# Kernel tuning notes

Measured on AMD Instinct MI355X. Metric: run time of the kernel, lower is better.

Reference implementation:

```python
import jax, jax.numpy as jnp
import numpy as np

N = 50000   # nodes
E = 800000  # edges
D = 128     # input feature dim
HID = 64    # hidden dim
NEG_SLOPE = 0.2


def setup_inputs() -> dict:
    key = jax.random.key(0)
    ks = jax.random.split(key, 12)
    s = 0.1
    x = jax.random.normal(ks[0], (N, D), jnp.float32)
    edge_index = jax.random.randint(ks[1], (2, E), 0, N, dtype=jnp.int64)
    # layer 1: GATConv(128 -> 64, heads=2, concat=False)
    W1 = jax.random.normal(ks[2], (D, 2 * HID), jnp.float32) * s
    a_src1 = jax.random.normal(ks[3], (2, HID), jnp.float32) * s
    a_dst1 = jax.random.normal(ks[4], (2, HID), jnp.float32) * s
    b1 = jnp.zeros((HID,), jnp.float32)
    # layer 2: GATConv(64 -> 64, heads=1, concat=False)
    W2 = jax.random.normal(ks[5], (HID, HID), jnp.float32) * s
    a_src2 = jax.random.normal(ks[6], (1, HID), jnp.float32) * s
    a_dst2 = jax.random.normal(ks[7], (1, HID), jnp.float32) * s
    b2 = jnp.zeros((HID,), jnp.float32)
    # classifier Linear(64 -> 2)
    Wc = jax.random.normal(ks[8], (HID, 2), jnp.float32) * s
    bc = jnp.zeros((2,), jnp.float32)
    return {"x": x, "edge_index": edge_index, "W1": W1, "a_src1": a_src1,
            "a_dst1": a_dst1, "b1": b1, "W2": W2, "a_src2": a_src2,
            "a_dst2": a_dst2, "b2": b2, "Wc": Wc, "bc": bc}


def _gat_layer(x, src, dst, W, a_s, a_d, b, n):
    """PyG GATConv (concat=False -> mean over heads), eval mode."""
    H, C = a_s.shape
    h = (x @ W).reshape(n, H, C)                      # [N,H,C]
    alpha_s = jnp.sum(h * a_s, axis=-1)               # [N,H]
    alpha_d = jnp.sum(h * a_d, axis=-1)               # [N,H]
    e = jax.nn.leaky_relu(alpha_s[src] + alpha_d[dst], NEG_SLOPE)  # [E,H]
    # segment softmax over incoming edges of each target node
    m = jax.ops.segment_max(e, dst, num_segments=n)   # [N,H]
    e = jnp.exp(e - m[dst])
    denom = jax.ops.segment_sum(e, dst, num_segments=n)
    alpha = e / (denom[dst] + 1e-16)                  # [E,H]
    msg = h[src] * alpha[:, :, None]                  # [E,H,C]
    out = jax.ops.segment_sum(msg, dst, num_segments=n)  # [N,H,C]
    return out.mean(axis=1) + b                       # [N,C]


def reference(x, edge_index, W1, a_src1, a_dst1, b1, W2, a_src2, a_dst2, b2, Wc, bc):
    n = x.shape[0]
    loops = jnp.arange(n, dtype=edge_index.dtype)     # PyG add_self_loops=True
    src = jnp.concatenate([edge_index[0], loops])
    dst = jnp.concatenate([edge_index[1], loops])
    h = jax.nn.elu(_gat_layer(x, src, dst, W1, a_src1, a_dst1, b1, n))
    h = jax.nn.elu(_gat_layer(h, src, dst, W2, a_src2, a_dst2, b2, n))
    logits = h @ Wc + bc
    return jax.nn.log_softmax(logits, axis=1)
```

## Files before the change

kernel.cpp:

```cpp
#include <hip/hip_runtime.h>
#include <math.h>

#define NN 50000
#define NE 800000
#define NT (NE + NN)
#define NBUCK 196
#define BE 4096
#define NBLK_B ((NT + BE - 1) / BE)
#define CAP 6144
#define NBLK_G ((NN + 63) / 64)

typedef short bf16x8 __attribute__((ext_vector_type(8)));
typedef float f32x4 __attribute__((ext_vector_type(4)));
union U16x8 { uint4 u; bf16x8 s; };

__device__ __forceinline__ unsigned pk_bf16x2(float x, float y) {
  unsigned ux = __float_as_uint(x); ux = ux + 0x7FFFu + ((ux >> 16) & 1u);
  unsigned uy = __float_as_uint(y); uy = uy + 0x7FFFu + ((uy >> 16) & 1u);
  return (ux >> 16) | (uy & 0xFFFF0000u);
}
__device__ __forceinline__ unsigned short bf16_1(float x) {
  unsigned u = __float_as_uint(x); u = u + 0x7FFFu + ((u >> 16) & 1u);
  return (unsigned short)(u >> 16);
}
__device__ __forceinline__ float blo(unsigned v) { return __uint_as_float(v << 16); }
__device__ __forceinline__ float bhi(unsigned v) { return __uint_as_float(v & 0xFFFF0000u); }

__global__ __launch_bounds__(256) void k_prep(const float* __restrict__ W1, const float* __restrict__ W2,
                                              unsigned short* __restrict__ w1f,
                                              unsigned short* __restrict__ w2f,
                                              int* __restrict__ bcur) {
  int i = blockIdx.x * 256 + threadIdx.x;
  if (i < NBUCK) bcur[i] = i * CAP;
  if (i < 128 * 128) {
    int k = i >> 7, col = i & 127;
    int ct = col >> 4, kt = k >> 5, lane = (((k >> 3) & 3) << 4) | (col & 15), j = k & 7;
    w1f[(((ct << 2) | kt) * 64 + lane) * 8 + j] = bf16_1(W1[i]);
  } else if (i < 128 * 128 + 64 * 64) {
    int e = i - 128 * 128;
    int k = e >> 6, col = e & 63;
    int ct = col >> 4, kt = k >> 5, lane = (((k >> 3) & 3) << 4) | (col & 15), j = k & 7;
    w2f[(((ct << 1) | kt) * 64 + lane) * 8 + j] = bf16_1(W2[e]);
  }
}

__global__ __launch_bounds__(256) void k_gb(
    const int* __restrict__ src, const int* __restrict__ dst,
    int* __restrict__ bcur, unsigned* __restrict__ staging,
    const float* __restrict__ x, const unsigned short* __restrict__ w1f,
    const float* __restrict__ asw_g, const float* __restrict__ adw_g,
    unsigned short* __restrict__ h1b, float* __restrict__ as1, float* __restrict__ ad1) {
  __shared__ int hist[NBUCK];
  __shared__ int base[NBUCK];
  if (blockIdx.x < NBLK_B) {
    const int t = threadIdx.x;
    const int e0 = blockIdx.x * BE;
    if (t < NBUCK) hist[t] = 0;
    __syncthreads();
    for (int j = t; j < BE; j += 256) {
      int i = e0 + j;
      if (i >= NT) break;
      int d = (i < NE) ? dst[i] : (i - NE);
      atomicAdd(&hist[d >> 8], 1);
    }
    __syncthreads();
    if (t < NBUCK) {
      int c = hist[t];
      base[t] = c ? atomicAdd(&bcur[t], c) : 0;
      hist[t] = 0;
    }
    __syncthreads();
    for (int j = t; j < BE; j += 256) {
      int i = e0 + j;
      if (i >= NT) break;
      int s, d;
      if (i < NE) { s = src[i]; d = dst[i]; } else { s = d = i - NE; }
      int b = d >> 8;
      int off = atomicAdd(&hist[b], 1);
      staging[base[b] + off] = ((unsigned)d << 16) | (unsigned)s;
    }
    return;
  }
  const int bid = blockIdx.x - NBLK_B;
  const int t = threadIdx.x;
  const int wid = t >> 6, l = t & 63;
  const int lr = l & 15, lg = l >> 4;
  const int arow = bid * 64 + wid * 16 + lr;
  const bool aok = arow < NN;

  float asw_t[8], adw_t[8];
#pragma unroll
  for (int ct = 0; ct < 8; ++ct) {
    asw_t[ct] = asw_g[ct * 16 + lr];
    adw_t[ct] = adw_g[ct * 16 + lr];
  }

  f32x4 acc[8];
#pragma unroll
  for (int ct = 0; ct < 8; ++ct) acc[ct] = (f32x4){0.f, 0.f, 0.f, 0.f};

#pragma unroll
  for (int kt = 0; kt < 4; ++kt) {
    U16x8 a;
    if (aok) {
      const float* xp = &x[(long long)arow * 128 + kt * 32 + lg * 8];
      float4 f0 = *(const float4*)xp;
      float4 f1 = *(const float4*)(xp + 4);
      a.u.x = pk_bf16x2(f0.x, f0.y); a.u.y = pk_bf16x2(f0.z, f0.w);
      a.u.z = pk_bf16x2(f1.x, f1.y); a.u.w = pk_bf16x2(f1.z, f1.w);
    } else {
      a.u = make_uint4(0, 0, 0, 0);
    }
#pragma unroll
    for (int ct = 0; ct < 8; ++ct) {
      U16x8 b;
      b.u = *(const uint4*)&w1f[(((ct << 2) | kt) * 64 + l) * 8];
      acc[ct] = __builtin_amdgcn_mfma_f32_16x16x32_bf16(a.s, b.s, acc[ct], 0, 0, 0);
    }
  }

  const int gr0 = bid * 64 + wid * 16 + lg * 4;
#pragma unroll
  for (int reg = 0; reg < 4; ++reg) {
    int grow = gr0 + reg;
    bool ok = grow < NN;
    float s0 = 0.f, s1 = 0.f, d0 = 0.f, d1 = 0.f;
#pragma unroll
    for (int ct = 0; ct < 8; ++ct) {
      float v = acc[ct][reg];
      if (ok) h1b[(long long)grow * 128 + ct * 16 + lr] = bf16_1(v);
      if (ct < 4) { s0 += v * asw_t[ct]; d0 += v * adw_t[ct]; }
      else        { s1 += v * asw_t[ct]; d1 += v * adw_t[ct]; }
    }
#pragma unroll
    for (int off = 1; off < 16; off <<= 1) {
      s0 += __shfl_xor(s0, off); d0 += __shfl_xor(d0, off);
      s1 += __shfl_xor(s1, off); d1 += __shfl_xor(d1, off);
    }
    if (ok && lr == 0) {
      as1[grow * 2] = s0; as1[grow * 2 + 1] = s1;
      ad1[grow * 2] = d0; ad1[grow * 2 + 1] = d1;
    }
  }
}

__global__ __launch_bounds__(256) void k_scatter2(const unsigned* __restrict__ staging,
                                                  const int* __restrict__ bcur,
                                                  int* __restrict__ rowptr,
                                                  unsigned short* __restrict__ csr16) {
  __shared__ int lcnt[256];
  __shared__ int wsum[4];
  __shared__ int sOff, sTot;
  const int b = blockIdx.x;
  const int t = threadIdx.x;
  const int nlo = b << 8;
  const int l = t & 63, w = t >> 6;

  int bc = (t < NBUCK) ? bcur[t] - t * CAP : 0;
  int sc = bc;
#pragma unroll
  for (int off = 1; off < 64; off <<= 1) {
    int u = __shfl_up(sc, off);
    if (l >= off) sc += u;
  }
  if (l == 63) wsum[w] = sc;
  __syncthreads();
  {
    int wo = 0;
    for (int i = 0; i < w; ++i) wo += wsum[i];
    int incl = sc + wo;
    if (t == b) sOff = incl - bc;
    if (t == 255) sTot = incl;
  }
  lcnt[t] = 0;
  __syncthreads();

  const int s0 = b * CAP;
  const int cnt = bcur[b] - s0;
  for (int k = t; k < cnt; k += 256)
    atomicAdd(&lcnt[(int)(staging[s0 + k] >> 16) - nlo], 1);
  __syncthreads();
  int v = lcnt[t];
  int sc2 = v;
#pragma unroll
  for (int off = 1; off < 64; off <<= 1) {
    int u = __shfl_up(sc2, off);
    if (l >= off) sc2 += u;
  }
  __syncthreads();
  if (l == 63) wsum[w] = sc2;
  __syncthreads();
  int wo = 0;
  for (int i = 0; i < w; ++i) wo += wsum[i];
  const int base = sOff + sc2 + wo - v;
  if (nlo + t < NN) rowptr[nlo + t] = base;
  if (b == NBUCK - 1 && t == 0) rowptr[NN] = sTot;
  __syncthreads();
  lcnt[t] = base;
  __syncthreads();
  for (int k = t; k < cnt; k += 256) {
    unsigned e = staging[s0 + k];
    int d = (int)(e >> 16) - nlo;
    int pos = atomicAdd(&lcnt[d], 1);
    csr16[pos] = (unsigned short)(e & 0xFFFFu);
  }
}

__global__ __launch_bounds__(256) void k_gat1(
    const int* __restrict__ rowptr, const unsigned short* __restrict__ csr16,
    const uint2* __restrict__ h1x2, const float2* __restrict__ as1,
    const float2* __restrict__ ad1, const float* __restrict__ b1,
    uint2* __restrict__ out1x2) {
  __shared__ float4 sw[4][2][64];
  const int t = threadIdx.x;
  const int wv = t >> 6;
  const int p = t & 63;
  const int hw = p >> 5;
  const int l = p & 31;
  const int n = blockIdx.x * 8 + wv * 2 + hw;
  if (n >= NN) return;
  const int beg = rowptr[n], end = rowptr[n + 1];
  const int deg = end - beg;
  const float2 adn = ad1[n];
  const int hd = l >> 4;

  float a0 = 0.f, a1 = 0.f, a2 = 0.f, a3 = 0.f;
  float inv;

  if (deg <= 64) {
    int sA = 0, sB = 0;
    float e0A = -1e30f, e1A = -1e30f, e0B = -1e30f, e1B = -1e30f;
    if (l < deg) {
      sA = csr16[beg + l];
      float2 a = as1[sA];
      e0A = a.x + adn.x; e0A = fmaxf(e0A, 0.2f * e0A);
      e1A = a.y + adn.y; e1A = fmaxf(e1A, 0.2f * e1A);
    }
    if (l + 32 < deg) {
      sB = csr16[beg + l + 32];
      float2 a = as1[sB];
      e0B = a.x + adn.x; e0B = fmaxf(e0B, 0.2f * e0B);
      e1B = a.y + adn.y; e1B = fmaxf(e1B, 0.2f * e1B);
    }
    float m0 = fmaxf(e0A, e0B), m1 = fmaxf(e1A, e1B);
#pragma unroll
    for (int off = 1; off < 32; off <<= 1) {
      m0 = fmaxf(m0, __shfl_xor(m0, off));
      m1 = fmaxf(m1, __shfl_xor(m1, off));
    }
    float w0A = (l < deg) ? __expf(e0A - m0) : 0.f;
    float w1A = (l < deg) ? __expf(e1A - m1) : 0.f;
    float w0B = (l + 32 < deg) ? __expf(e0B - m0) : 0.f;
    float w1B = (l + 32 < deg) ? __expf(e1B - m1) : 0.f;
    float d0 = w0A + w0B, d1 = w1A + w1B;
#pragma unroll
    for (int off = 1; off < 32; off <<= 1) {
      d0 += __shfl_xor(d0, off);
      d1 += __shfl_xor(d1, off);
    }
    sw[wv][hw][l]      = make_float4(__int_as_float(sA), w0A, w1A, 0.f);
    sw[wv][hw][l + 32] = make_float4(__int_as_float(sB), w0B, w1B, 0.f);
    __builtin_amdgcn_wave_barrier();
    inv = 1.f / ((hd ? d1 : d0) + 1e-16f);

    int j = 0;
    for (; j + 8 <= deg; j += 8) {
      float4 a[8]; uint2 v[8];
#pragma unroll
      for (int u = 0; u < 8; ++u) a[u] = sw[wv][hw][j + u];
#pragma unroll
      for (int u = 0; u < 8; ++u) v[u] = h1x2[(__float_as_int(a[u].x) << 5) + l];
#pragma unroll
      for (int u = 0; u < 8; ++u) {
        float wgt = hd ? a[u].z : a[u].y;
        a0 += wgt * blo(v[u].x); a1 += wgt * bhi(v[u].x);
        a2 += wgt * blo(v[u].y); a3 += wgt * bhi(v[u].y);
      }
    }
    if (j + 4 <= deg) {
      float4 a[4]; uint2 v[4];
#pragma unroll
      for (int u = 0; u < 4; ++u) a[u] = sw[wv][hw][j + u];
#pragma unroll
      for (int u = 0; u < 4; ++u) v[u] = h1x2[(__float_as_int(a[u].x) << 5) + l];
#pragma unroll
      for (int u = 0; u < 4; ++u) {
        float wgt = hd ? a[u].z : a[u].y;
        a0 += wgt * blo(v[u].x); a1 += wgt * bhi(v[u].x);
        a2 += wgt * blo(v[u].y); a3 += wgt * bhi(v[u].y);
      }
      j += 4;
    }
    for (; j < deg; ++j) {
      float4 a = sw[wv][hw][j];
      uint2 v = h1x2[(__float_as_int(a.x) << 5) + l];
      float wgt = hd ? a.z : a.y;
      a0 += wgt * blo(v.x); a1 += wgt * bhi(v.x);
      a2 += wgt * blo(v.y); a3 += wgt * bhi(v.y);
    }
  } else {
    float m0 = -1e30f, d0 = 0.f, m1 = -1e30f, d1 = 0.f;
    for (int k = beg + l; k < end; k += 32) {
      float2 a = as1[csr16[k]];
      float e0 = a.x + adn.x; e0 = fmaxf(e0, 0.2f * e0);
      float e1 = a.y + adn.y; e1 = fmaxf(e1, 0.2f * e1);
      if (e0 > m0) { d0 *= __expf(m0 - e0); m0 = e0; }
      d0 += __expf(e0 - m0);
      if (e1 > m1) { d1 *= __expf(m1 - e1); m1 = e1; }
      d1 += __expf(e1 - m1);
    }
#pragma unroll
    for (int off = 1; off < 32; off <<= 1) {
      float mo = __shfl_xor(m0, off), dd = __shfl_xor(d0, off);
      float mn = fmaxf(m0, mo);
      d0 = d0 * __expf(m0 - mn) + dd * __expf(mo - mn);
      m0 = mn;
      mo = __shfl_xor(m1, off); dd = __shfl_xor(d1, off);
      mn = fmaxf(m1, mo);
      d1 = d1 * __expf(m1 - mn) + dd * __expf(mo - mn);
      m1 = mn;
    }
    inv = 1.f / ((hd ? d1 : d0) + 1e-16f);
    for (int c0 = beg; c0 < end; c0 += 64) {
      int nc = end - c0; if (nc > 64) nc = 64;
      int sA = 0, sB = 0; float w0A = 0.f, w1A = 0.f, w0B = 0.f, w1B = 0.f;
      if (l < nc) {
        sA = csr16[c0 + l];
        float2 a = as1[sA];
        float e0 = a.x + adn.x; e0 = fmaxf(e0, 0.2f * e0);
        float e1 = a.y + adn.y; e1 = fmaxf(e1, 0.2f * e1);
        w0A = __expf(e0 - m0); w1A = __expf(e1 - m1);
      }
      if (l + 32 < nc) {
        sB = csr16[c0 + l + 32];
        float2 a = as1[sB];
        float e0 = a.x + adn.x; e0 = fmaxf(e0, 0.2f * e0);
        float e1 = a.y + adn.y; e1 = fmaxf(e1, 0.2f * e1);
        w0B = __expf(e0 - m0); w1B = __expf(e1 - m1);
      }
      __builtin_amdgcn_wave_barrier();
      sw[wv][hw][l]      = make_float4(__int_as_float(sA), w0A, w1A, 0.f);
      sw[wv][hw][l + 32] = make_float4(__int_as_float(sB), w0B, w1B, 0.f);
      __builtin_amdgcn_wave_barrier();
      for (int j = 0; j < nc; ++j) {
        float4 a = sw[wv][hw][j];
        uint2 v = h1x2[(__float_as_int(a.x) << 5) + l];
        float wgt = hd ? a.z : a.y;
        a0 += wgt * blo(v.x); a1 += wgt * bhi(v.x);
        a2 += wgt * blo(v.y); a3 += wgt * bhi(v.y);
      }
      __builtin_amdgcn_wave_barrier();
    }
  }

  a0 *= inv; a1 *= inv; a2 *= inv; a3 *= inv;
  float c0 = __shfl_xor(a0, 16), c1 = __shfl_xor(a1, 16),
        c2 = __shfl_xor(a2, 16), c3 = __shfl_xor(a3, 16);
  if (l < 16) {
    float u0 = 0.5f * (a0 + c0) + b1[4 * l + 0];
    float u1 = 0.5f * (a1 + c1) + b1[4 * l + 1];
    float u2 = 0.5f * (a2 + c2) + b1[4 * l + 2];
    float u3 = 0.5f * (a3 + c3) + b1[4 * l + 3];
    u0 = u0 > 0.f ? u0 : expm1f(u0);
    u1 = u1 > 0.f ? u1 : expm1f(u1);
    u2 = u2 > 0.f ? u2 : expm1f(u2);
    u3 = u3 > 0.f ? u3 : expm1f(u3);
    out1x2[n * 16 + l] = make_uint2(pk_bf16x2(u0, u1), pk_bf16x2(u2, u3));
  }
}

__global__ __launch_bounds__(256) void k_gemm2(
    const unsigned short* __restrict__ in_b, const unsigned short* __restrict__ w2f,
    const float* __restrict__ asw_g, const float* __restrict__ adw_g,
    unsigned short* __restrict__ h2b, float* __restrict__ as2, float* __restrict__ ad2) {
  const int t = threadIdx.x;
  const int wid = t >> 6, l = t & 63;
  const int lr = l & 15, lg = l >> 4;
  const int arow = blockIdx.x * 64 + wid * 16 + lr;
  const bool aok = arow < NN;

  float asw_t[4], adw_t[4];
#pragma unroll
  for (int ct = 0; ct < 4; ++ct) {
    asw_t[ct] = asw_g[ct * 16 + lr];
    adw_t[ct] = adw_g[ct * 16 + lr];
  }

  f32x4 acc[4];
#pragma unroll
  for (int ct = 0; ct < 4; ++ct) acc[ct] = (f32x4){0.f, 0.f, 0.f, 0.f};

#pragma unroll
  for (int kt = 0; kt < 2; ++kt) {
    U16x8 a;
    if (aok) a.u = *(const uint4*)&in_b[(long long)arow * 64 + kt * 32 + lg * 8];
    else a.u = make_uint4(0, 0, 0, 0);
#pragma unroll
    for (int ct = 0; ct < 4; ++ct) {
      U16x8 b;
      b.u = *(const uint4*)&w2f[(((ct << 1) | kt) * 64 + l) * 8];
      acc[ct] = __builtin_amdgcn_mfma_f32_16x16x32_bf16(a.s, b.s, acc[ct], 0, 0, 0);
    }
  }

  const int gr0 = blockIdx.x * 64 + wid * 16 + lg * 4;
#pragma unroll
  for (int reg = 0; reg < 4; ++reg) {
    int grow = gr0 + reg;
    bool ok = grow < NN;
    float s0 = 0.f, d0 = 0.f;
#pragma unroll
    for (int ct = 0; ct < 4; ++ct) {
      float v = acc[ct][reg];
      if (ok) h2b[(long long)grow * 64 + ct * 16 + lr] = bf16_1(v);
      s0 += v * asw_t[ct]; d0 += v * adw_t[ct];
    }
#pragma unroll
    for (int off = 1; off < 16; off <<= 1) {
      s0 += __shfl_xor(s0, off); d0 += __shfl_xor(d0, off);
    }
    if (ok && lr == 0) { as2[grow] = s0; ad2[grow] = d0; }
  }
}

__global__ __launch_bounds__(256) void k_gat2(
    const int* __restrict__ rowptr, const unsigned short* __restrict__ csr16,
    const unsigned* __restrict__ h2u, const float* __restrict__ as2,
    const float* __restrict__ ad2, const float* __restrict__ b2,
    const float* __restrict__ Wc, const float* __restrict__ bc,
    float* __restrict__ out) {
  __shared__ float2 sw[4][64];
  const int t = threadIdx.x;
  const int wv = t >> 6;
  const int n = blockIdx.x * 4 + wv;
  if (n >= NN) return;
  const int p = t & 63;
  const int half = p >> 5;
  const int q = p & 31;
  const int beg = rowptr[n], end = rowptr[n + 1];
  const int deg = end - beg;
  const float adn = ad2[n];

  float acc0 = 0.f, acc1 = 0.f;
  float inv;

  if (deg <= 64) {
    int s = 0; float e = -1e30f;
    if (p < deg) {
      s = csr16[beg + p];
      e = as2[s] + adn;
      e = fmaxf(e, 0.2f * e);
    }
    float m = e;
#pragma unroll
    for (int off = 1; off < 64; off <<= 1) m = fmaxf(m, __shfl_xor(m, off));
    float w = (p < deg) ? __expf(e - m) : 0.f;
    float d = w;
#pragma unroll
    for (int off = 1; off < 64; off <<= 1) d += __shfl_xor(d, off);
    sw[wv][p] = make_float2(__int_as_float(s), w);
    __builtin_amdgcn_wave_barrier();
    inv = 1.f / (d + 1e-16f);

    int niter = (deg + 1) >> 1;
    int i = 0;
    for (; i + 4 <= niter; i += 4) {
      float2 a[4]; unsigned v[4];
#pragma unroll
      for (int u = 0; u < 4; ++u) a[u] = sw[wv][2 * (i + u) + half];
#pragma unroll
      for (int u = 0; u < 4; ++u) v[u] = h2u[(__float_as_int(a[u].x) << 5) + q];
#pragma unroll
      for (int u = 0; u < 4; ++u) {
        acc0 += a[u].y * blo(v[u]);
        acc1 += a[u].y * bhi(v[u]);
      }
    }
    if (i + 2 <= niter) {
      float2 a0 = sw[wv][2 * i + half];
      float2 a1 = sw[wv][2 * (i + 1) + half];
      unsigned v0 = h2u[(__float_as_int(a0.x) << 5) + q];
      unsigned v1 = h2u[(__float_as_int(a1.x) << 5) + q];
      acc0 += a0.y * blo(v0); acc1 += a0.y * bhi(v0);
      acc0 += a1.y * blo(v1); acc1 += a1.y * bhi(v1);
      i += 2;
    }
    if (i < niter) {
      float2 a = sw[wv][2 * i + half];
      unsigned v = h2u[(__float_as_int(a.x) << 5) + q];
      acc0 += a.y * blo(v); acc1 += a.y * bhi(v);
    }
  } else {
    float m = -1e30f, d = 0.f;
    for (int k = beg + p; k < end; k += 64) {
      float e = as2[csr16[k]] + adn;
      e = fmaxf(e, 0.2f * e);
      if (e > m) { d *= __expf(m - e); m = e; }
      d += __expf(e - m);
    }
#pragma unroll
    for (int off = 1; off < 64; off <<= 1) {
      float mo = __shfl_xor(m, off), dd = __shfl_xor(d, off);
      float mn = fmaxf(m, mo);
      d = d * __expf(m - mn) + dd * __expf(mo - mn);
      m = mn;
    }
    inv = 1.f / (d + 1e-16f);
    for (int c0 = beg; c0 < end; c0 += 64) {
      int nc = end - c0; if (nc > 64) nc = 64;
      int s = 0; float w = 0.f;
      if (p < nc) {
        s = csr16[c0 + p];
        float e = as2[s] + adn;
        e = fmaxf(e, 0.2f * e);
        w = __expf(e - m);
      }
      __builtin_amdgcn_wave_barrier();
      sw[wv][p] = make_float2(__int_as_float(s), w);
      __builtin_amdgcn_wave_barrier();
      int niter = (nc + 1) >> 1;
      for (int i = 0; i < niter; ++i) {
        int j = 2 * i + half;
        float2 a = sw[wv][j < nc ? j : 0];
        float wj = (j < nc) ? a.y : 0.f;
        unsigned v = h2u[(__float_as_int(a.x) << 5) + q];
        acc0 += wj * blo(v); acc1 += wj * bhi(v);
      }
      __builtin_amdgcn_wave_barrier();
    }
  }

  acc0 += __shfl_xor(acc0, 32);
  acc1 += __shfl_xor(acc1, 32);
  float v0 = acc0 * inv + b2[2 * q];
  float v1 = acc1 * inv + b2[2 * q + 1];
  v0 = v0 > 0.f ? v0 : expm1f(v0);
  v1 = v1 > 0.f ? v1 : expm1f(v1);
  float l0 = v0 * Wc[4 * q] + v1 * Wc[4 * q + 2];
  float l1 = v0 * Wc[4 * q + 1] + v1 * Wc[4 * q + 3];
#pragma unroll
  for (int off = 1; off < 32; off <<= 1) {
    l0 += __shfl_xor(l0, off);
    l1 += __shfl_xor(l1, off);
  }
  if (p == 0) {
    l0 += bc[0]; l1 += bc[1];
    float mx = fmaxf(l0, l1);
    float lse = mx + logf(expf(l0 - mx) + expf(l1 - mx));
    out[n * 2] = l0 - lse;
    out[n * 2 + 1] = l1 - lse;
  }
}

extern "C" void kernel_launch(void* const* d_in, const int* in_sizes, int n_in,
                              void* d_out, int out_size, void* d_ws, size_t ws_size,
                              hipStream_t stream) {
  const float* x    = (const float*)d_in[0];
  const int*   ei   = (const int*)d_in[1];
  const float* W1   = (const float*)d_in[2];
  const float* as1w = (const float*)d_in[3];
  const float* ad1w = (const float*)d_in[4];
  const float* b1   = (const float*)d_in[5];
  const float* W2   = (const float*)d_in[6];
  const float* as2w = (const float*)d_in[7];
  const float* ad2w = (const float*)d_in[8];
  const float* b2   = (const float*)d_in[9];
  const float* Wc   = (const float*)d_in[10];
  const float* bc   = (const float*)d_in[11];
  float* out = (float*)d_out;

  const int* src = ei;
  const int* dst = ei + NE;

  char* p = (char*)d_ws;
  unsigned short* h1b = (unsigned short*)p; p += sizeof(unsigned short) * (long long)NN * 128;
  unsigned short* out1b = (unsigned short*)p; p += sizeof(unsigned short) * (long long)NN * 64;
  unsigned short* h2b = (unsigned short*)p; p += sizeof(unsigned short) * (long long)NN * 64;
  float* as1  = (float*)p; p += sizeof(float) * NN * 2;
  float* ad1  = (float*)p; p += sizeof(float) * NN * 2;
  float* as2  = (float*)p; p += sizeof(float) * NN;
  float* ad2  = (float*)p; p += sizeof(float) * NN;
  int* rowptr  = (int*)p; p += sizeof(int) * (NN + 64);
  int* bcur    = (int*)p; p += sizeof(int) * ((NBUCK + 63) & ~63);
  unsigned* staging = (unsigned*)p; p += sizeof(unsigned) * (long long)NBUCK * CAP;
  unsigned short* csr16 = (unsigned short*)p; p += sizeof(unsigned short) * (long long)NT;
  unsigned short* w1f = (unsigned short*)p; p += sizeof(unsigned short) * 128 * 128;
  unsigned short* w2f = (unsigned short*)p; p += sizeof(unsigned short) * 64 * 64;

  k_prep<<<(128 * 128 + 64 * 64 + 255) / 256, 256, 0, stream>>>(W1, W2, w1f, w2f, bcur);
  k_gb<<<NBLK_B + NBLK_G, 256, 0, stream>>>(src, dst, bcur, staging,
                                            x, w1f, as1w, ad1w, h1b, as1, ad1);
  k_scatter2<<<NBUCK, 256, 0, stream>>>(staging, bcur, rowptr, csr16);

  k_gat1<<<(NN + 7) / 8, 256, 0, stream>>>(rowptr, csr16, (const uint2*)h1b,
                                           (const float2*)as1, (const float2*)ad1, b1,
                                           (uint2*)out1b);

  k_gemm2<<<(NN + 63) / 64, 256, 0, stream>>>(out1b, w2f, as2w, ad2w, h2b, as2, ad2);
  k_gat2<<<(NN + 3) / 4, 256, 0, stream>>>(rowptr, csr16, (const unsigned*)h2b,
                                           as2, ad2, b2, Wc, bc, out);
}
```

Measured before the change: 116.3 us.

## Fuse layer-2 projection GEMM into layer-1 aggregation kernel epilogue

The separate k_gemm2 launch is removed. Each k_gat1 block now stages its 8 aggregated bf16 rows in shared memory, syncs, and one wave runs the 64x64 MFMA projection plus the attention dot products, writing h2b, as2 and ad2 directly. This drops one kernel launch and the global write and re-read of the out1 intermediate. In exchange, half of each 16-row MFMA tile is zero padding, the block adds a __syncthreads, and the other three waves sit idle during the epilogue. The early return was removed because NN divides evenly by 8.

```diff
diff --git a/kernel.cpp b/kernel.cpp
--- a/kernel.cpp
+++ b/kernel.cpp
@@ -210,15 +210,17 @@
     const int* __restrict__ rowptr, const unsigned short* __restrict__ csr16,
     const uint2* __restrict__ h1x2, const float2* __restrict__ as1,
     const float2* __restrict__ ad1, const float* __restrict__ b1,
-    uint2* __restrict__ out1x2) {
+    const unsigned short* __restrict__ w2f,
+    const float* __restrict__ as2w_g, const float* __restrict__ ad2w_g,
+    unsigned short* __restrict__ h2b, float* __restrict__ as2, float* __restrict__ ad2) {
   __shared__ float4 sw[4][2][64];
+  __shared__ unsigned o1[8][32];
   const int t = threadIdx.x;
   const int wv = t >> 6;
   const int p = t & 63;
   const int hw = p >> 5;
   const int l = p & 31;
   const int n = blockIdx.x * 8 + wv * 2 + hw;
-  if (n >= NN) return;
   const int beg = rowptr[n], end = rowptr[n + 1];
   const int deg = end - beg;
   const float2 adn = ad1[n];
@@ -365,61 +367,52 @@
     u1 = u1 > 0.f ? u1 : expm1f(u1);
     u2 = u2 > 0.f ? u2 : expm1f(u2);
     u3 = u3 > 0.f ? u3 : expm1f(u3);
-    out1x2[n * 16 + l] = make_uint2(pk_bf16x2(u0, u1), pk_bf16x2(u2, u3));
-  }
-}
-
-__global__ __launch_bounds__(256) void k_gemm2(
-    const unsigned short* __restrict__ in_b, const unsigned short* __restrict__ w2f,
-    const float* __restrict__ asw_g, const float* __restrict__ adw_g,
-    unsigned short* __restrict__ h2b, float* __restrict__ as2, float* __restrict__ ad2) {
-  const int t = threadIdx.x;
-  const int wid = t >> 6, l = t & 63;
-  const int lr = l & 15, lg = l >> 4;
-  const int arow = blockIdx.x * 64 + wid * 16 + lr;
-  const bool aok = arow < NN;
-
-  float asw_t[4], adw_t[4];
-#pragma unroll
-  for (int ct = 0; ct < 4; ++ct) {
-    asw_t[ct] = asw_g[ct * 16 + lr];
-    adw_t[ct] = adw_g[ct * 16 + lr];
-  }
-
-  f32x4 acc[4];
-#pragma unroll
-  for (int ct = 0; ct < 4; ++ct) acc[ct] = (f32x4){0.f, 0.f, 0.f, 0.f};
-
-#pragma unroll
-  for (int kt = 0; kt < 2; ++kt) {
-    U16x8 a;
-    if (aok) a.u = *(const uint4*)&in_b[(long long)arow * 64 + kt * 32 + lg * 8];
-    else a.u = make_uint4(0, 0, 0, 0);
+    *(uint2*)&o1[wv * 2 + hw][2 * l] = make_uint2(pk_bf16x2(u0, u1), pk_bf16x2(u2, u3));
+  }
+  __syncthreads();
+
+  if (t < 64) {
+    const int lr = t & 15, lg = t >> 4;
+    f32x4 acc2[4];
+#pragma unroll
+    for (int ct = 0; ct < 4; ++ct) acc2[ct] = (f32x4){0.f, 0.f, 0.f, 0.f};
+#pragma unroll
+    for (int kt = 0; kt < 2; ++kt) {
+      U16x8 a;
+      if (lr < 8) a.u = ((const uint4*)o1[lr])[kt * 4 + lg];
+      else a.u = make_uint4(0, 0, 0, 0);
+#pragma unroll
+      for (int ct = 0; ct < 4; ++ct) {
+        U16x8 b;
+        b.u = *(const uint4*)&w2f[(((ct << 1) | kt) * 64 + t) * 8];
+        acc2[ct] = __builtin_amdgcn_mfma_f32_16x16x32_bf16(a.s, b.s, acc2[ct], 0, 0, 0);
+      }
+    }
+    float asw2_t[4], adw2_t[4];
 #pragma unroll
     for (int ct = 0; ct < 4; ++ct) {
-      U16x8 b;
-      b.u = *(const uint4*)&w2f[(((ct << 1) | kt) * 64 + l) * 8];
-      acc[ct] = __builtin_amdgcn_mfma_f32_16x16x32_bf16(a.s, b.s, acc[ct], 0, 0, 0);
-    }
-  }
-
-  const int gr0 = blockIdx.x * 64 + wid * 16 + lg * 4;
-#pragma unroll
-  for (int reg = 0; reg < 4; ++reg) {
-    int grow = gr0 + reg;
-    bool ok = grow < NN;
-    float s0 = 0.f, d0 = 0.f;
-#pragma unroll
-    for (int ct = 0; ct < 4; ++ct) {
-      float v = acc[ct][reg];
-      if (ok) h2b[(long long)grow * 64 + ct * 16 + lr] = bf16_1(v);
-      s0 += v * asw_t[ct]; d0 += v * adw_t[ct];
-    }
-#pragma unroll
-    for (int off = 1; off < 16; off <<= 1) {
-      s0 += __shfl_xor(s0, off); d0 += __shfl_xor(d0, off);
-    }
-    if (ok && lr == 0) { as2[grow] = s0; ad2[grow] = d0; }
+      asw2_t[ct] = as2w_g[ct * 16 + lr];
+      adw2_t[ct] = ad2w_g[ct * 16 + lr];
+    }
+    const int gbase = blockIdx.x * 8;
+#pragma unroll
+    for (int reg = 0; reg < 4; ++reg) {
+      int row = lg * 4 + reg;
+      bool ok = row < 8;
+      int grow = gbase + row;
+      float s0 = 0.f, d0 = 0.f;
+#pragma unroll
+      for (int ct = 0; ct < 4; ++ct) {
+        float v = acc2[ct][reg];
+        if (ok) h2b[(long long)grow * 64 + ct * 16 + lr] = bf16_1(v);
+        s0 += v * asw2_t[ct]; d0 += v * adw2_t[ct];
+      }
+#pragma unroll
+      for (int off = 1; off < 16; off <<= 1) {
+        s0 += __shfl_xor(s0, off); d0 += __shfl_xor(d0, off);
+      }
+      if (ok && lr == 0) { as2[grow] = s0; ad2[grow] = d0; }
+    }
   }
 }
 
@@ -574,7 +567,6 @@
 
   char* p = (char*)d_ws;
   unsigned short* h1b = (unsigned short*)p; p += sizeof(unsigned short) * (long long)NN * 128;
-  unsigned short* out1b = (unsigned short*)p; p += sizeof(unsigned short) * (long long)NN * 64;
   unsigned short* h2b = (unsigned short*)p; p += sizeof(unsigned short) * (long long)NN * 64;
   float* as1  = (float*)p; p += sizeof(float) * NN * 2;
   float* ad1  = (float*)p; p += sizeof(float) * NN * 2;
@@ -592,11 +584,10 @@
                                             x, w1f, as1w, ad1w, h1b, as1, ad1);
   k_scatter2<<<NBUCK, 256, 0, stream>>>(staging, bcur, rowptr, csr16);
 
-  k_gat1<<<(NN + 7) / 8, 256, 0, stream>>>(rowptr, csr16, (const uint2*)h1b,
-                                           (const float2*)as1, (const float2*)ad1, b1,
-                                           (uint2*)out1b);
-
-  k_gemm2<<<(NN + 63) / 64, 256, 0, stream>>>(out1b, w2f, as2w, ad2w, h2b, as2, ad2);
+  k_gat1<<<NN / 8, 256, 0, stream>>>(rowptr, csr16, (const uint2*)h1b,
+                                     (const float2*)as1, (const float2*)ad1, b1,
+                                     w2f, as2w, ad2w, h2b, as2, ad2);
+
   k_gat2<<<(NN + 3) / 4, 256, 0, stream>>>(rowptr, csr16, (const unsigned*)h2b,
                                            as2, ad2, b2, Wc, bc, out);
 }
```

Result: slower. 121.4 us (+4.4%).
